# Kernel optimization log

Hardware: AMD Instinct MI355X
Metric: run time of the kernel (lower is better)

The kernel has to match this reference:

```python
import jax, jax.numpy as jnp
import numpy as np

D_MODEL = 1792
BB = 256
I = D_MODEL + BB  # inner_dim = 2048


def setup_inputs() -> dict:
    key = jax.random.key(0)
    ks = jax.random.split(key, 10)
    s = 1.0 / np.sqrt(I)  # PyTorch LSTM default init range
    u = lambda k, shape: jax.random.uniform(k, shape, jnp.float32, -s, s)
    return {
        "x": jax.random.normal(ks[0], (6, D_MODEL), jnp.float32),
        "y": jax.random.normal(ks[1], (5, BB), jnp.float32),
        "Wih5": u(ks[2], (5, 4 * I, I)),
        "Whh5": u(ks[3], (5, 4 * I, I)),
        "bih5": u(ks[4], (5, 4 * I)),
        "bhh5": u(ks[5], (5, 4 * I)),
        "WihF": u(ks[6], (4 * I, D_MODEL)),
        "WhhF": u(ks[7], (4 * I, I)),
        "bihF": u(ks[8], (4 * I,)),
        "bhhF": u(ks[9], (4 * I,)),
    }


def _cell(h, c, xt, Wih, Whh, bih, bhh):
    # PyTorch LSTM cell: gates in i, f, g, o order
    g = Wih @ xt + bih + Whh @ h + bhh  # (4I,)
    i, f, gg, o = jnp.split(g, 4)
    c = jax.nn.sigmoid(f) * c + jax.nn.sigmoid(i) * jnp.tanh(gg)
    h = jax.nn.sigmoid(o) * jnp.tanh(c)
    return h, c


def reference(x, y, Wih5, Whh5, bih5, bhh5, WihF, WhhF, bihF, bhhF):
    # inpt: (5, inner_dim) = concat of first 5 frames and 5 gts
    inpt = jnp.concatenate([x[:-1], y], axis=1)
    h0 = jnp.zeros((I,), x.dtype)
    c0 = jnp.zeros((I,), x.dtype)

    def step(carry, xs):
        h, c = carry
        xt, Wih, Whh, bih, bhh = xs
        return _cell(h, c, xt, Wih, Whh, bih, bhh), None

    # 5 sequential single-step LSTM cells (distinct weights), fused via scan
    (h, c), _ = jax.lax.scan(step, (h0, c0), (inpt, Wih5, Whh5, bih5, bhh5))
    # final LSTM consumes the last frame (d_model input)
    h, c = _cell(h, c, x[-1], WihF, WhhF, bihF, bhhF)
    return h[-BB:]
```

## Files before the change

### kernel.cpp

```cpp
#include <hip/hip_runtime.h>
#include <cmath>

#define D_MODEL 1792
#define BB      256
#define II      2048
#define FOURI   8192

__device__ __forceinline__ float sigm(float v) { return 1.0f / (1.0f + expf(-v)); }

__device__ __forceinline__ float waveReduce(float s) {
    #pragma unroll
    for (int off = 32; off > 0; off >>= 1) s += __shfl_down(s, off, 64);
    return s;
}

__global__ __launch_bounds__(256) void ih_kernel(
    const float* __restrict__ x,
    const float* __restrict__ y,
    const float* __restrict__ Wih5,
    const float* __restrict__ bih5,
    const float* __restrict__ bhh5,
    const float* __restrict__ WihF,
    const float* __restrict__ bihF,
    const float* __restrict__ bhhF,
    float* __restrict__ gih)
{
    const int blk  = blockIdx.x;
    const int wave = threadIdx.x >> 6;
    const int lane = threadIdx.x & 63;

    if (blk < 10240) {
        const int t = blk >> 11;
        const int r = ((blk & 2047) << 2) + wave;
        const float* wrow = Wih5 + ((size_t)t * FOURI + r) * (size_t)II;
        const float* xt = x + t * D_MODEL;
        const float* yt = y + t * BB;
        float sum = 0.f;
        #pragma unroll
        for (int p = 0; p < 8; ++p) {
            const int j = p * 256 + lane * 4;
            float4 w = *(const float4*)(wrow + j);
            float4 v = (p < 7) ? *(const float4*)(xt + j)
                               : *(const float4*)(yt + (j - D_MODEL));
            sum += w.x * v.x + w.y * v.y + w.z * v.z + w.w * v.w;
        }
        sum = waveReduce(sum);
        if (lane == 0)
            gih[t * FOURI + r] = sum + bih5[t * FOURI + r] + bhh5[t * FOURI + r];
    } else {
        const int u = (blk - 10240) * 4 + wave;
        const int q = u >> 8;
        const int k = u & 255;
        const int r = q * II + D_MODEL + k;
        const float* wrow = WihF + (size_t)r * (size_t)D_MODEL;
        const float* x5 = x + 5 * D_MODEL;
        float sum = 0.f;
        #pragma unroll
        for (int p = 0; p < 7; ++p) {
            const int j = p * 256 + lane * 4;
            float4 w = *(const float4*)(wrow + j);
            float4 v = *(const float4*)(x5 + j);
            sum += w.x * v.x + w.y * v.y + w.z * v.z + w.w * v.w;
        }
        sum = waveReduce(sum);
        if (lane == 0)
            gih[5 * FOURI + r] = sum + bihF[r] + bhhF[r];
    }
}

__global__ __launch_bounds__(256) void step0_kernel(
    const float* __restrict__ gih,
    float* __restrict__ h_out,
    float* __restrict__ c_out)
{
    const int r = blockIdx.x * 256 + threadIdx.x;
    const float gi = gih[r];
    const float gg = gih[2 * II + r];
    const float go = gih[3 * II + r];
    const float cc = sigm(gi) * tanhf(gg);
    c_out[r] = cc;
    h_out[r] = sigm(go) * tanhf(cc);
}

__global__ __launch_bounds__(256) void hh_step_kernel(
    const float* __restrict__ Whh,
    const float* __restrict__ gih_t,
    const float* __restrict__ h_in,
    float* __restrict__ h_out,
    float* __restrict__ c)
{
    __shared__ float partial[4];
    const int r    = blockIdx.x;
    const int wave = threadIdx.x >> 6;
    const int lane = threadIdx.x & 63;

    const float* wrow = Whh + ((size_t)wave * II + r) * (size_t)II;
    float sum = 0.f;
    #pragma unroll
    for (int p = 0; p < 8; ++p) {
        const int j = p * 256 + lane * 4;
        float4 w = *(const float4*)(wrow + j);
        float4 v = *(const float4*)(h_in + j);
        sum += w.x * v.x + w.y * v.y + w.z * v.z + w.w * v.w;
    }
    sum = waveReduce(sum);
    if (lane == 0) partial[wave] = sum + gih_t[wave * II + r];
    __syncthreads();
    if (threadIdx.x == 0) {
        const float gi = partial[0], gf = partial[1], gg = partial[2], go = partial[3];
        const float cc = sigm(gf) * c[r] + sigm(gi) * tanhf(gg);
        c[r] = cc;
        h_out[r] = sigm(go) * tanhf(cc);
    }
}

__global__ __launch_bounds__(256) void final_kernel(
    const float* __restrict__ WhhF,
    const float* __restrict__ gihF,
    const float* __restrict__ h_in,
    const float* __restrict__ c,
    float* __restrict__ out)
{
    __shared__ float partial[4];
    const int k    = blockIdx.x;
    const int r    = D_MODEL + k;
    const int wave = threadIdx.x >> 6;
    const int lane = threadIdx.x & 63;

    const float* wrow = WhhF + ((size_t)wave * II + r) * (size_t)II;
    float sum = 0.f;
    #pragma unroll
    for (int p = 0; p < 8; ++p) {
        const int j = p * 256 + lane * 4;
        float4 w = *(const float4*)(wrow + j);
        float4 v = *(const float4*)(h_in + j);
        sum += w.x * v.x + w.y * v.y + w.z * v.z + w.w * v.w;
    }
    sum = waveReduce(sum);
    if (lane == 0) partial[wave] = sum + gihF[wave * II + r];
    __syncthreads();
    if (threadIdx.x == 0) {
        const float gi = partial[0], gf = partial[1], gg = partial[2], go = partial[3];
        const float cc = sigm(gf) * c[r] + sigm(gi) * tanhf(gg);
        out[k] = sigm(go) * tanhf(cc);
    }
}

extern "C" void kernel_launch(void* const* d_in, const int* in_sizes, int n_in,
                              void* d_out, int out_size, void* d_ws, size_t ws_size,
                              hipStream_t stream) {
    const float* x    = (const float*)d_in[0];
    const float* y    = (const float*)d_in[1];
    const float* Wih5 = (const float*)d_in[2];
    const float* Whh5 = (const float*)d_in[3];
    const float* bih5 = (const float*)d_in[4];
    const float* bhh5 = (const float*)d_in[5];
    const float* WihF = (const float*)d_in[6];
    const float* WhhF = (const float*)d_in[7];
    const float* bihF = (const float*)d_in[8];
    const float* bhhF = (const float*)d_in[9];
    float* out = (float*)d_out;

    float* ws   = (float*)d_ws;
    float* gih  = ws;
    float* hA   = ws + 6 * FOURI;
    float* hB   = hA + II;
    float* cbuf = hB + II;

    ih_kernel<<<10496, 256, 0, stream>>>(x, y, Wih5, bih5, bhh5, WihF, bihF, bhhF, gih);

    step0_kernel<<<II / 256, 256, 0, stream>>>(gih, hA, cbuf);

    const float* hin = hA;
    float* hout = hB;
    for (int t = 1; t <= 4; ++t) {
        hh_step_kernel<<<II, 256, 0, stream>>>(
            Whh5 + (size_t)t * FOURI * II, gih + t * FOURI, hin, hout, cbuf);
        float* tmp = hout;
        hout = (float*)hin;
        hin = tmp;
    }

    final_kernel<<<BB, 256, 0, stream>>>(WhhF, gih + 5 * FOURI, hin, cbuf, out);
}
```

Measured before the change: 120.1 us.

## Fuse next-step input projections into each recurrent LSTM step kernel

After: 121.0 us. No clear change (+0.7%).

```diff
diff --git a/kernel.cpp b/kernel.cpp
--- a/kernel.cpp
+++ b/kernel.cpp
@@ -14,46 +14,148 @@
     return s;
 }
 
-__global__ __launch_bounds__(256) void ih_kernel(
+__device__ __forceinline__ float dotConcat(const float* __restrict__ wrow,
+                                           const float* __restrict__ xt,
+                                           const float* __restrict__ yt,
+                                           int lane) {
+    float sum = 0.f;
+    #pragma unroll
+    for (int p = 0; p < 8; ++p) {
+        const int j = p * 256 + lane * 4;
+        float4 w = *(const float4*)(wrow + j);
+        float4 v = (p < 7) ? *(const float4*)(xt + j)
+                           : *(const float4*)(yt + (j - D_MODEL));
+        sum += w.x * v.x + w.y * v.y + w.z * v.z + w.w * v.w;
+    }
+    return sum;
+}
+
+__device__ __forceinline__ float dotH(const float* __restrict__ wrow,
+                                      const float* __restrict__ h,
+                                      int lane) {
+    float sum = 0.f;
+    #pragma unroll
+    for (int p = 0; p < 8; ++p) {
+        const int j = p * 256 + lane * 4;
+        float4 w = *(const float4*)(wrow + j);
+        float4 v = *(const float4*)(h + j);
+        sum += w.x * v.x + w.y * v.y + w.z * v.z + w.w * v.w;
+    }
+    return sum;
+}
+
+__global__ __launch_bounds__(256) void step0_kernel(
     const float* __restrict__ x,
     const float* __restrict__ y,
     const float* __restrict__ Wih5,
     const float* __restrict__ bih5,
     const float* __restrict__ bhh5,
+    float* __restrict__ h_out,
+    float* __restrict__ c_out,
+    float* __restrict__ gih_out)
+{
+    const int wave = threadIdx.x >> 6;
+    const int lane = threadIdx.x & 63;
+
+    if (blockIdx.x < 2048) {
+        __shared__ float partial[4];
+        const int r = blockIdx.x;
+        const float* wrow = Wih5 + ((size_t)wave * II + r) * (size_t)II;
+        float sum = dotConcat(wrow, x, y, lane);
+        sum = waveReduce(sum);
+        if (lane == 0)
+            partial[wave] = sum + bih5[wave * II + r] + bhh5[wave * II + r];
+        __syncthreads();
+        if (threadIdx.x == 0) {
+            const float gi = partial[0], gg = partial[2], go = partial[3];
+            const float cc = sigm(gi) * tanhf(gg);
+            c_out[r] = cc;
+            h_out[r] = sigm(go) * tanhf(cc);
+        }
+    } else {
+        const int u = blockIdx.x - 2048;
+        const float* wrow = Wih5 + ((size_t)FOURI + (size_t)wave * II + u) * (size_t)II;
+        float sum = dotConcat(wrow, x + D_MODEL, y + BB, lane);
+        sum = waveReduce(sum);
+        if (lane == 0)
+            gih_out[wave * II + u] =
+                sum + bih5[FOURI + wave * II + u] + bhh5[FOURI + wave * II + u];
+    }
+}
+
+__global__ __launch_bounds__(256) void mid_kernel(
+    const float* __restrict__ Whh,
+    const float* __restrict__ gih_in,
+    const float* __restrict__ h_in,
+    float* __restrict__ h_out,
+    float* __restrict__ c,
+    const float* __restrict__ WihN,
+    const float* __restrict__ bihN,
+    const float* __restrict__ bhhN,
+    const float* __restrict__ xN,
+    const float* __restrict__ yN,
+    float* __restrict__ gih_out)
+{
+    const int wave = threadIdx.x >> 6;
+    const int lane = threadIdx.x & 63;
+
+    if (blockIdx.x < 2048) {
+        __shared__ float partial[4];
+        const int r = blockIdx.x;
+        const float* wrow = Whh + ((size_t)wave * II + r) * (size_t)II;
+        float sum = dotH(wrow, h_in, lane);
+        sum = waveReduce(sum);
+        if (lane == 0) partial[wave] = sum + gih_in[wave * II + r];
+        __syncthreads();
+        if (threadIdx.x == 0) {
+            const float gi = partial[0], gf = partial[1], gg = partial[2], go = partial[3];
+            const float cc = sigm(gf) * c[r] + sigm(gi) * tanhf(gg);
+            c[r] = cc;
+            h_out[r] = sigm(go) * tanhf(cc);
+        }
+    } else {
+        const int u = blockIdx.x - 2048;
+        const float* wrow = WihN + ((size_t)wave * II + u) * (size_t)II;
+        float sum = dotConcat(wrow, xN, yN, lane);
+        sum = waveReduce(sum);
+        if (lane == 0)
+            gih_out[wave * II + u] = sum + bihN[wave * II + u] + bhhN[wave * II + u];
+    }
+}
+
+__global__ __launch_bounds__(256) void mid4_kernel(
+    const float* __restrict__ Whh,
+    const float* __restrict__ gih_in,
+    const float* __restrict__ h_in,
+    float* __restrict__ h_out,
+    float* __restrict__ c,
     const float* __restrict__ WihF,
     const float* __restrict__ bihF,
     const float* __restrict__ bhhF,
-    float* __restrict__ gih)
-{
-    const int blk  = blockIdx.x;
-    const int wave = threadIdx.x >> 6;
-    const int lane = threadIdx.x & 63;
-
-    if (blk < 10240) {
-        const int t = blk >> 11;
-        const int r = ((blk & 2047) << 2) + wave;
-        const float* wrow = Wih5 + ((size_t)t * FOURI + r) * (size_t)II;
-        const float* xt = x + t * D_MODEL;
-        const float* yt = y + t * BB;
-        float sum = 0.f;
-        #pragma unroll
-        for (int p = 0; p < 8; ++p) {
-            const int j = p * 256 + lane * 4;
-            float4 w = *(const float4*)(wrow + j);
-            float4 v = (p < 7) ? *(const float4*)(xt + j)
-                               : *(const float4*)(yt + (j - D_MODEL));
-            sum += w.x * v.x + w.y * v.y + w.z * v.z + w.w * v.w;
-        }
-        sum = waveReduce(sum);
-        if (lane == 0)
-            gih[t * FOURI + r] = sum + bih5[t * FOURI + r] + bhh5[t * FOURI + r];
+    const float* __restrict__ x5,
+    float* __restrict__ gihF_out)
+{
+    const int wave = threadIdx.x >> 6;
+    const int lane = threadIdx.x & 63;
+
+    if (blockIdx.x < 2048) {
+        __shared__ float partial[4];
+        const int r = blockIdx.x;
+        const float* wrow = Whh + ((size_t)wave * II + r) * (size_t)II;
+        float sum = dotH(wrow, h_in, lane);
+        sum = waveReduce(sum);
+        if (lane == 0) partial[wave] = sum + gih_in[wave * II + r];
+        __syncthreads();
+        if (threadIdx.x == 0) {
+            const float gi = partial[0], gf = partial[1], gg = partial[2], go = partial[3];
+            const float cc = sigm(gf) * c[r] + sigm(gi) * tanhf(gg);
+            c[r] = cc;
+            h_out[r] = sigm(go) * tanhf(cc);
+        }
     } else {
-        const int u = (blk - 10240) * 4 + wave;
-        const int q = u >> 8;
-        const int k = u & 255;
-        const int r = q * II + D_MODEL + k;
+        const int u = blockIdx.x - 2048;
+        const int r = wave * II + D_MODEL + u;
         const float* wrow = WihF + (size_t)r * (size_t)D_MODEL;
-        const float* x5 = x + 5 * D_MODEL;
         float sum = 0.f;
         #pragma unroll
         for (int p = 0; p < 7; ++p) {
@@ -64,53 +166,7 @@
         }
         sum = waveReduce(sum);
         if (lane == 0)
-            gih[5 * FOURI + r] = sum + bihF[r] + bhhF[r];
-    }
-}
-
-__global__ __launch_bounds__(256) void step0_kernel(
-    const float* __restrict__ gih,
-    float* __restrict__ h_out,
-    float* __restrict__ c_out)
-{
-    const int r = blockIdx.x * 256 + threadIdx.x;
-    const float gi = gih[r];
-    const float gg = gih[2 * II + r];
-    const float go = gih[3 * II + r];
-    const float cc = sigm(gi) * tanhf(gg);
-    c_out[r] = cc;
-    h_out[r] = sigm(go) * tanhf(cc);
-}
-
-__global__ __launch_bounds__(256) void hh_step_kernel(
-    const float* __restrict__ Whh,
-    const float* __restrict__ gih_t,
-    const float* __restrict__ h_in,
-    float* __restrict__ h_out,
-    float* __restrict__ c)
-{
-    __shared__ float partial[4];
-    const int r    = blockIdx.x;
-    const int wave = threadIdx.x >> 6;
-    const int lane = threadIdx.x & 63;
-
-    const float* wrow = Whh + ((size_t)wave * II + r) * (size_t)II;
-    float sum = 0.f;
-    #pragma unroll
-    for (int p = 0; p < 8; ++p) {
-        const int j = p * 256 + lane * 4;
-        float4 w = *(const float4*)(wrow + j);
-        float4 v = *(const float4*)(h_in + j);
-        sum += w.x * v.x + w.y * v.y + w.z * v.z + w.w * v.w;
-    }
-    sum = waveReduce(sum);
-    if (lane == 0) partial[wave] = sum + gih_t[wave * II + r];
-    __syncthreads();
-    if (threadIdx.x == 0) {
-        const float gi = partial[0], gf = partial[1], gg = partial[2], go = partial[3];
-        const float cc = sigm(gf) * c[r] + sigm(gi) * tanhf(gg);
-        c[r] = cc;
-        h_out[r] = sigm(go) * tanhf(cc);
+            gihF_out[wave * BB + u] = sum + bihF[r] + bhhF[r];
     }
 }
 
@@ -128,16 +184,9 @@
     const int lane = threadIdx.x & 63;
 
     const float* wrow = WhhF + ((size_t)wave * II + r) * (size_t)II;
-    float sum = 0.f;
-    #pragma unroll
-    for (int p = 0; p < 8; ++p) {
-        const int j = p * 256 + lane * 4;
-        float4 w = *(const float4*)(wrow + j);
-        float4 v = *(const float4*)(h_in + j);
-        sum += w.x * v.x + w.y * v.y + w.z * v.z + w.w * v.w;
-    }
+    float sum = dotH(wrow, h_in, lane);
     sum = waveReduce(sum);
-    if (lane == 0) partial[wave] = sum + gihF[wave * II + r];
+    if (lane == 0) partial[wave] = sum + gihF[wave * BB + k];
     __syncthreads();
     if (threadIdx.x == 0) {
         const float gi = partial[0], gf = partial[1], gg = partial[2], go = partial[3];
@@ -162,24 +211,35 @@
     float* out = (float*)d_out;
 
     float* ws   = (float*)d_ws;
-    float* gih  = ws;
-    float* hA   = ws + 6 * FOURI;
+    float* gihA = ws;
+    float* gihB = gihA + FOURI;
+    float* gihF = gihB + FOURI;
+    float* hA   = gihF + 1024;
     float* hB   = hA + II;
     float* cbuf = hB + II;
 
-    ih_kernel<<<10496, 256, 0, stream>>>(x, y, Wih5, bih5, bhh5, WihF, bihF, bhhF, gih);
-
-    step0_kernel<<<II / 256, 256, 0, stream>>>(gih, hA, cbuf);
-
-    const float* hin = hA;
-    float* hout = hB;
-    for (int t = 1; t <= 4; ++t) {
-        hh_step_kernel<<<II, 256, 0, stream>>>(
-            Whh5 + (size_t)t * FOURI * II, gih + t * FOURI, hin, hout, cbuf);
-        float* tmp = hout;
-        hout = (float*)hin;
-        hin = tmp;
-    }
-
-    final_kernel<<<BB, 256, 0, stream>>>(WhhF, gih + 5 * FOURI, hin, cbuf, out);
-}
+    const size_t WOFF = (size_t)FOURI * II;
+
+    step0_kernel<<<4096, 256, 0, stream>>>(x, y, Wih5, bih5, bhh5, hA, cbuf, gihA);
+
+    mid_kernel<<<4096, 256, 0, stream>>>(
+        Whh5 + 1 * WOFF, gihA, hA, hB, cbuf,
+        Wih5 + 2 * WOFF, bih5 + 2 * FOURI, bhh5 + 2 * FOURI,
+        x + 2 * D_MODEL, y + 2 * BB, gihB);
+
+    mid_kernel<<<4096, 256, 0, stream>>>(
+        Whh5 + 2 * WOFF, gihB, hB, hA, cbuf,
+        Wih5 + 3 * WOFF, bih5 + 3 * FOURI, bhh5 + 3 * FOURI,
+        x + 3 * D_MODEL, y + 3 * BB, gihA);
+
+    mid_kernel<<<4096, 256, 0, stream>>>(
+        Whh5 + 3 * WOFF, gihA, hA, hB, cbuf,
+        Wih5 + 4 * WOFF, bih5 + 4 * FOURI, bhh5 + 4 * FOURI,
+        x + 4 * D_MODEL, y + 4 * BB, gihB);
+
+    mid4_kernel<<<2304, 256, 0, stream>>>(
+        Whh5 + 4 * WOFF, gihB, hB, hA, cbuf,
+        WihF, bihF, bhhF, x + 5 * D_MODEL, gihF);
+
+    final_kernel<<<BB, 256, 0, stream>>>(WhhF, gihF, hA, cbuf, out);
+}
```
